# Kernel tuning notes

Hardware: AMD Instinct MI355X
Metric: run time of the kernel (lower is better)

Reference implementation:

```python
import jax, jax.numpy as jnp
import numpy as np

HEAD_DIM = 128
HIDDEN = 2048
MAX_SEQ = 2048
NUM_HEADS = 16
NUM_KV_HEADS = 8
NUM_LAYERS = 32
LAYER_IDX = 5
SCALE = 1.0 / HEAD_DIM ** 0.5
N_REP = NUM_HEADS // NUM_KV_HEADS


def setup_inputs() -> dict:
    key = jax.random.key(0)
    ks = jax.random.split(key, 6)
    x = jax.random.normal(ks[0], (1, HIDDEN, 1, 1), jnp.float32)
    kv_cache = jax.random.normal(ks[1], (2 * NUM_LAYERS, NUM_KV_HEADS, MAX_SEQ, HEAD_DIM), jnp.float32)
    q_w = jax.random.normal(ks[2], (NUM_HEADS * HEAD_DIM, HIDDEN), jnp.float32) * 0.02
    k_w = jax.random.normal(ks[3], (NUM_KV_HEADS * HEAD_DIM, HIDDEN), jnp.float32) * 0.02
    v_w = jax.random.normal(ks[4], (NUM_KV_HEADS * HEAD_DIM, HIDDEN), jnp.float32) * 0.02
    o_w = jax.random.normal(ks[5], (HIDDEN, NUM_HEADS * HEAD_DIM), jnp.float32) * 0.02
    return {"x": x, "kv_cache": kv_cache, "q_w": q_w, "k_w": k_w, "v_w": v_w,
            "o_w": o_w, "current_pos": 1024}


def reference(x, kv_cache, q_w, k_w, v_w, o_w, current_pos):
    # 1x1 Conv2d on [1, C, 1, 1] == matrix-vector product
    xv = x.reshape(HIDDEN)
    q = (q_w @ xv).reshape(NUM_HEADS, HEAD_DIM)        # [H, D]
    k = (k_w @ xv).reshape(NUM_KV_HEADS, HEAD_DIM)     # [KV, D]
    v = (v_w @ xv).reshape(NUM_KV_HEADS, HEAD_DIM)     # [KV, D]

    k_idx = 2 * LAYER_IDX
    v_idx = k_idx + 1
    # functional slice-write of the new token's K/V into the cache
    kv_cache = kv_cache.at[k_idx, :, current_pos, :].set(k)
    kv_cache = kv_cache.at[v_idx, :, current_pos, :].set(v)

    k_full = kv_cache[k_idx]   # [KV, S, D]
    v_full = kv_cache[v_idx]   # [KV, S, D]

    # GQA: q head h uses kv head h // N_REP (matches repeat+view in torch)
    qg = q.reshape(NUM_KV_HEADS, N_REP, HEAD_DIM)                     # [KV, R, D]
    scores = jnp.einsum('grd,gsd->grs', qg, k_full) * SCALE           # [KV, R, S]
    probs = jax.nn.softmax(scores, axis=-1)
    attn = jnp.einsum('grs,gsd->grd', probs, v_full)                  # [KV, R, D]
    attn = attn.reshape(NUM_HEADS * HEAD_DIM)

    out = (o_w @ attn).reshape(1, HIDDEN, 1, 1)
    return out
```

## Files before the change

### kernel.cpp

```cpp
#include <hip/hip_runtime.h>

#define HEAD_DIM   128
#define HIDDEN     2048
#define MAX_SEQ    2048
#define NUM_HEADS  16
#define NUM_KV     8
#define LAYER_IDX  5
#define NSPLIT     16
#define CHUNK      128
#define SCALE      0.08838834764831845f

#define WS_Q     0
#define WS_K     2048
#define WS_V     3072
#define WS_LP    4096
#define WS_OP    4352

__device__ __forceinline__ float wave_reduce_sum(float v) {
    #pragma unroll
    for (int off = 32; off > 0; off >>= 1) v += __shfl_xor(v, off);
    return v;
}

__global__ __launch_bounds__(256) void qkv_kernel(const float* __restrict__ x,
                                                  const float* __restrict__ q_w,
                                                  const float* __restrict__ k_w,
                                                  const float* __restrict__ v_w,
                                                  float* __restrict__ ws) {
    const int t  = threadIdx.x;
    const int r0 = blockIdx.x * 4;
    float4 x0 = ((const float4*)x)[t];
    float4 x1 = ((const float4*)x)[t + 256];

    const float* w0; int obase; float s_out;
    if (r0 < 2048)      { w0 = q_w + (size_t)r0 * HIDDEN;          obase = WS_Q + r0;          s_out = SCALE; }
    else if (r0 < 3072) { w0 = k_w + (size_t)(r0 - 2048) * HIDDEN; obase = WS_K + (r0 - 2048); s_out = 1.0f; }
    else                { w0 = v_w + (size_t)(r0 - 3072) * HIDDEN; obase = WS_V + (r0 - 3072); s_out = 1.0f; }

    float p[4];
    #pragma unroll
    for (int r = 0; r < 4; ++r) {
        const float* w = w0 + (size_t)r * HIDDEN;
        float4 a0 = ((const float4*)w)[t];
        float4 a1 = ((const float4*)w)[t + 256];
        p[r] = a0.x * x0.x + a0.y * x0.y + a0.z * x0.z + a0.w * x0.w
             + a1.x * x1.x + a1.y * x1.y + a1.z * x1.z + a1.w * x1.w;
    }
    #pragma unroll
    for (int r = 0; r < 4; ++r) p[r] = wave_reduce_sum(p[r]);

    __shared__ float red[4][4];
    const int wave = t >> 6, lane = t & 63;
    if (lane == 0) {
        #pragma unroll
        for (int r = 0; r < 4; ++r) red[r][wave] = p[r];
    }
    __syncthreads();
    if (t < 4) ws[obase + t] = (red[t][0] + red[t][1] + red[t][2] + red[t][3]) * s_out;
}

__global__ __launch_bounds__(256) void attn_kernel(const float* __restrict__ kv_cache,
                                                   const float* __restrict__ wsq,
                                                   const int* __restrict__ cur_pos,
                                                   float* __restrict__ lp,
                                                   float* __restrict__ op) {
    const int g     = blockIdx.x;
    const int split = blockIdx.y;
    const int s0    = split * CHUNK;
    const int cpos  = *cur_pos;
    const int t     = threadIdx.x;
    const int wave  = t >> 6, lane = t & 63;

    const float* kbase = kv_cache + ((size_t)(2 * LAYER_IDX)     * NUM_KV + g) * (size_t)MAX_SEQ * HEAD_DIM;
    const float* vbase = kv_cache + ((size_t)(2 * LAYER_IDX + 1) * NUM_KV + g) * (size_t)MAX_SEQ * HEAD_DIM;
    const float* knew  = wsq + WS_K + g * HEAD_DIM;
    const float* vnew  = wsq + WS_V + g * HEAD_DIM;

    __shared__ float4 tile[CHUNK * 32];
    __shared__ float  sc[2][CHUNK];
    __shared__ float4 smv[2][8][32];
    __shared__ float  lred[2][2];
    __shared__ float  lsum[2];

    const int dq = lane & 3;
    float4 q0s[8], q1s[8];
    {
        const float4* q04 = (const float4*)(wsq + WS_Q + (g * 2 + 0) * HEAD_DIM);
        const float4* q14 = (const float4*)(wsq + WS_Q + (g * 2 + 1) * HEAD_DIM);
        #pragma unroll
        for (int r = 0; r < 8; ++r) { q0s[r] = q04[dq * 8 + r]; q1s[r] = q14[dq * 8 + r]; }
    }

    #pragma unroll
    for (int i = 0; i < 16; ++i) {
        const int idx = i * 256 + t;
        const int row = idx >> 5, col = idx & 31;
        const int s = s0 + row;
        const float4* src = (s == cpos) ? (const float4*)knew
                                        : (const float4*)(kbase + (size_t)s * HEAD_DIM);
        tile[idx] = src[col];
    }
    __syncthreads();

    #pragma unroll
    for (int p = 0; p < 2; ++p) {
        const int pos = p * 64 + wave * 16 + (lane >> 2);
        float a0 = 0.f, a1 = 0.f;
        #pragma unroll
        for (int r = 0; r < 8; ++r) {
            float4 kk = tile[pos * 32 + dq * 8 + r];
            a0 += q0s[r].x * kk.x + q0s[r].y * kk.y + q0s[r].z * kk.z + q0s[r].w * kk.w;
            a1 += q1s[r].x * kk.x + q1s[r].y * kk.y + q1s[r].z * kk.z + q1s[r].w * kk.w;
        }
        a0 += __shfl_xor(a0, 1); a0 += __shfl_xor(a0, 2);
        a1 += __shfl_xor(a1, 1); a1 += __shfl_xor(a1, 2);
        if (dq == 0) { sc[0][pos] = a0; sc[1][pos] = a1; }
    }
    __syncthreads();

    if (t < 128) {
        float e0 = __expf(sc[0][t]);
        float e1 = __expf(sc[1][t]);
        sc[0][t] = e0; sc[1][t] = e1;
        float w0 = wave_reduce_sum(e0);
        float w1 = wave_reduce_sum(e1);
        if (lane == 0) { lred[0][wave] = w0; lred[1][wave] = w1; }
    }
    __syncthreads();
    if (t == 0) {
        lsum[0] = lred[0][0] + lred[0][1];
        lsum[1] = lred[1][0] + lred[1][1];
    }

    __syncthreads();
    #pragma unroll
    for (int i = 0; i < 16; ++i) {
        const int idx = i * 256 + t;
        const int row = idx >> 5, col = idx & 31;
        const int s = s0 + row;
        const float4* src = (s == cpos) ? (const float4*)vnew
                                        : (const float4*)(vbase + (size_t)s * HEAD_DIM);
        tile[idx] = src[col];
    }
    __syncthreads();

    {
        const int d4 = t & 31, subrow = t >> 5;
        float4 a0 = {0.f,0.f,0.f,0.f}, a1 = {0.f,0.f,0.f,0.f};
        #pragma unroll
        for (int i = 0; i < 16; ++i) {
            const int j = i * 8 + subrow;
            float4 vv = tile[j * 32 + d4];
            const float e0 = sc[0][j], e1 = sc[1][j];
            a0.x += e0 * vv.x; a0.y += e0 * vv.y; a0.z += e0 * vv.z; a0.w += e0 * vv.w;
            a1.x += e1 * vv.x; a1.y += e1 * vv.y; a1.z += e1 * vv.z; a1.w += e1 * vv.w;
        }
        smv[0][subrow][d4] = a0;
        smv[1][subrow][d4] = a1;
    }
    __syncthreads();
    if (t < 64) {
        const int rep = t >> 5, q4 = t & 31;
        float4 s = smv[rep][0][q4];
        #pragma unroll
        for (int r = 1; r < 8; ++r) {
            float4 b = smv[rep][r][q4];
            s.x += b.x; s.y += b.y; s.z += b.z; s.w += b.w;
        }
        const int h = g * 2 + rep;
        ((float4*)(op + ((size_t)(h * NSPLIT + split)) * HEAD_DIM))[q4] = s;
    }
    if (t == 0) {
        lp[(g * 2 + 0) * NSPLIT + split] = lsum[0];
        lp[(g * 2 + 1) * NSPLIT + split] = lsum[1];
    }
}

__global__ __launch_bounds__(256) void out_kernel(const float* __restrict__ o_w,
                                                  const float* __restrict__ lp,
                                                  const float* __restrict__ op,
                                                  float* __restrict__ out) {
    const int t = threadIdx.x;
    __shared__ float  linv[NUM_HEADS];
    __shared__ float4 attn_s[512];
    __shared__ float  red[8][4];

    if (t < NUM_HEADS) {
        float l = 0.f;
        #pragma unroll
        for (int s = 0; s < NSPLIT; ++s) l += lp[t * NSPLIT + s];
        linv[t] = 1.0f / l;
    }
    __syncthreads();

    const float4* op4 = (const float4*)op;
    #pragma unroll
    for (int k = 0; k < 2; ++k) {
        const int fi = t + 256 * k;
        const int h = fi >> 5, d4 = fi & 31;
        float4 acc = {0.f,0.f,0.f,0.f};
        #pragma unroll
        for (int s = 0; s < NSPLIT; ++s) {
            float4 v = op4[(h * NSPLIT + s) * 32 + d4];
            acc.x += v.x; acc.y += v.y; acc.z += v.z; acc.w += v.w;
        }
        const float li = linv[h];
        acc.x *= li; acc.y *= li; acc.z *= li; acc.w *= li;
        attn_s[fi] = acc;
    }
    __syncthreads();

    const int row0 = blockIdx.x * 8;
    float4 xa0 = attn_s[t];
    float4 xa1 = attn_s[t + 256];

    float p[8];
    #pragma unroll
    for (int r = 0; r < 8; ++r) {
        const float* w = o_w + (size_t)(row0 + r) * HIDDEN;
        float4 a0 = ((const float4*)w)[t];
        float4 a1 = ((const float4*)w)[t + 256];
        p[r] = a0.x * xa0.x + a0.y * xa0.y + a0.z * xa0.z + a0.w * xa0.w
             + a1.x * xa1.x + a1.y * xa1.y + a1.z * xa1.z + a1.w * xa1.w;
    }
    #pragma unroll
    for (int r = 0; r < 8; ++r) p[r] = wave_reduce_sum(p[r]);

    const int wave = t >> 6, lane = t & 63;
    if (lane == 0) {
        #pragma unroll
        for (int r = 0; r < 8; ++r) red[r][wave] = p[r];
    }
    __syncthreads();
    if (t < 8) out[row0 + t] = red[t][0] + red[t][1] + red[t][2] + red[t][3];
}

extern "C" void kernel_launch(void* const* d_in, const int* in_sizes, int n_in,
                              void* d_out, int out_size, void* d_ws, size_t ws_size,
                              hipStream_t stream) {
    const float* x    = (const float*)d_in[0];
    const float* kv   = (const float*)d_in[1];
    const float* q_w  = (const float*)d_in[2];
    const float* k_w  = (const float*)d_in[3];
    const float* v_w  = (const float*)d_in[4];
    const float* o_w  = (const float*)d_in[5];
    const int*   cpos = (const int*)d_in[6];
    float* ws  = (float*)d_ws;
    float* out = (float*)d_out;

    qkv_kernel<<<1024, 256, 0, stream>>>(x, q_w, k_w, v_w, ws);
    attn_kernel<<<dim3(NUM_KV, NSPLIT), 256, 0, stream>>>(kv, ws, cpos, ws + WS_LP, ws + WS_OP);
    out_kernel<<<256, 256, 0, stream>>>(o_w, ws + WS_LP, ws + WS_OP, out);
}
```

Before: 25.43 us.

## Stream K/V directly from global in attention, widen blocks, double QKV rows per block

The attention kernel drops the shared-memory K and V tiles and has each thread read its K row and V rows straight from global memory, running 512 threads per block so the 128 positions are covered in one pass. This removes two tile-staging phases and their barriers, and lets the V loads start without waiting for a full tile copy. The QKV projection now computes 8 rows per block over half as many blocks, and the output kernel reduces the split sums with shuffles instead of a serial loop. The trade-offs are that K and V reads are now less coalesced across the wave and the QKV kernel has fewer blocks, which lowers occupancy.

```diff
diff --git a/kernel.cpp b/kernel.cpp
--- a/kernel.cpp
+++ b/kernel.cpp
@@ -28,7 +28,7 @@
                                                   const float* __restrict__ v_w,
                                                   float* __restrict__ ws) {
     const int t  = threadIdx.x;
-    const int r0 = blockIdx.x * 4;
+    const int r0 = blockIdx.x * 8;
     float4 x0 = ((const float4*)x)[t];
     float4 x1 = ((const float4*)x)[t + 256];
 
@@ -37,9 +37,9 @@
     else if (r0 < 3072) { w0 = k_w + (size_t)(r0 - 2048) * HIDDEN; obase = WS_K + (r0 - 2048); s_out = 1.0f; }
     else                { w0 = v_w + (size_t)(r0 - 3072) * HIDDEN; obase = WS_V + (r0 - 3072); s_out = 1.0f; }
 
-    float p[4];
-    #pragma unroll
-    for (int r = 0; r < 4; ++r) {
+    float p[8];
+    #pragma unroll
+    for (int r = 0; r < 8; ++r) {
         const float* w = w0 + (size_t)r * HIDDEN;
         float4 a0 = ((const float4*)w)[t];
         float4 a1 = ((const float4*)w)[t + 256];
@@ -47,19 +47,19 @@
              + a1.x * x1.x + a1.y * x1.y + a1.z * x1.z + a1.w * x1.w;
     }
     #pragma unroll
-    for (int r = 0; r < 4; ++r) p[r] = wave_reduce_sum(p[r]);
-
-    __shared__ float red[4][4];
+    for (int r = 0; r < 8; ++r) p[r] = wave_reduce_sum(p[r]);
+
+    __shared__ float red[8][4];
     const int wave = t >> 6, lane = t & 63;
     if (lane == 0) {
         #pragma unroll
-        for (int r = 0; r < 4; ++r) red[r][wave] = p[r];
-    }
-    __syncthreads();
-    if (t < 4) ws[obase + t] = (red[t][0] + red[t][1] + red[t][2] + red[t][3]) * s_out;
-}
-
-__global__ __launch_bounds__(256) void attn_kernel(const float* __restrict__ kv_cache,
+        for (int r = 0; r < 8; ++r) red[r][wave] = p[r];
+    }
+    __syncthreads();
+    if (t < 8) ws[obase + t] = (red[t][0] + red[t][1] + red[t][2] + red[t][3]) * s_out;
+}
+
+__global__ __launch_bounds__(512) void attn_kernel(const float* __restrict__ kv_cache,
                                                    const float* __restrict__ wsq,
                                                    const int* __restrict__ cur_pos,
                                                    float* __restrict__ lp,
@@ -76,41 +76,26 @@
     const float* knew  = wsq + WS_K + g * HEAD_DIM;
     const float* vnew  = wsq + WS_V + g * HEAD_DIM;
 
-    __shared__ float4 tile[CHUNK * 32];
     __shared__ float  sc[2][CHUNK];
-    __shared__ float4 smv[2][8][32];
-    __shared__ float  lred[2][2];
-    __shared__ float  lsum[2];
-
-    const int dq = lane & 3;
-    float4 q0s[8], q1s[8];
+    __shared__ float4 smv[2][16][32];
+    __shared__ float  lred4[4];
+
     {
+        const int dq  = lane & 3;
+        const int pos = wave * 16 + (lane >> 2);
+        const int s   = s0 + pos;
+        const float4* krow = (s == cpos) ? (const float4*)knew
+                                         : (const float4*)(kbase + (size_t)s * HEAD_DIM);
         const float4* q04 = (const float4*)(wsq + WS_Q + (g * 2 + 0) * HEAD_DIM);
         const float4* q14 = (const float4*)(wsq + WS_Q + (g * 2 + 1) * HEAD_DIM);
-        #pragma unroll
-        for (int r = 0; r < 8; ++r) { q0s[r] = q04[dq * 8 + r]; q1s[r] = q14[dq * 8 + r]; }
-    }
-
-    #pragma unroll
-    for (int i = 0; i < 16; ++i) {
-        const int idx = i * 256 + t;
-        const int row = idx >> 5, col = idx & 31;
-        const int s = s0 + row;
-        const float4* src = (s == cpos) ? (const float4*)knew
-                                        : (const float4*)(kbase + (size_t)s * HEAD_DIM);
-        tile[idx] = src[col];
-    }
-    __syncthreads();
-
-    #pragma unroll
-    for (int p = 0; p < 2; ++p) {
-        const int pos = p * 64 + wave * 16 + (lane >> 2);
         float a0 = 0.f, a1 = 0.f;
         #pragma unroll
         for (int r = 0; r < 8; ++r) {
-            float4 kk = tile[pos * 32 + dq * 8 + r];
-            a0 += q0s[r].x * kk.x + q0s[r].y * kk.y + q0s[r].z * kk.z + q0s[r].w * kk.w;
-            a1 += q1s[r].x * kk.x + q1s[r].y * kk.y + q1s[r].z * kk.z + q1s[r].w * kk.w;
+            float4 kk = krow[dq * 8 + r];
+            float4 qa = q04[dq * 8 + r];
+            float4 qb = q14[dq * 8 + r];
+            a0 += qa.x * kk.x + qa.y * kk.y + qa.z * kk.z + qa.w * kk.w;
+            a1 += qb.x * kk.x + qb.y * kk.y + qb.z * kk.z + qb.w * kk.w;
         }
         a0 += __shfl_xor(a0, 1); a0 += __shfl_xor(a0, 2);
         a1 += __shfl_xor(a1, 1); a1 += __shfl_xor(a1, 2);
@@ -118,29 +103,12 @@
     }
     __syncthreads();
 
-    if (t < 128) {
-        float e0 = __expf(sc[0][t]);
-        float e1 = __expf(sc[1][t]);
-        sc[0][t] = e0; sc[1][t] = e1;
-        float w0 = wave_reduce_sum(e0);
-        float w1 = wave_reduce_sum(e1);
-        if (lane == 0) { lred[0][wave] = w0; lred[1][wave] = w1; }
-    }
-    __syncthreads();
-    if (t == 0) {
-        lsum[0] = lred[0][0] + lred[0][1];
-        lsum[1] = lred[1][0] + lred[1][1];
-    }
-
-    __syncthreads();
-    #pragma unroll
-    for (int i = 0; i < 16; ++i) {
-        const int idx = i * 256 + t;
-        const int row = idx >> 5, col = idx & 31;
-        const int s = s0 + row;
-        const float4* src = (s == cpos) ? (const float4*)vnew
-                                        : (const float4*)(vbase + (size_t)s * HEAD_DIM);
-        tile[idx] = src[col];
+    if (t < 256) {
+        const int rr = t >> 7, j = t & 127;
+        float e = __expf(sc[rr][j]);
+        sc[rr][j] = e;
+        float l = wave_reduce_sum(e);
+        if (lane == 0) lred4[wave] = l;
     }
     __syncthreads();
 
@@ -148,9 +116,11 @@
         const int d4 = t & 31, subrow = t >> 5;
         float4 a0 = {0.f,0.f,0.f,0.f}, a1 = {0.f,0.f,0.f,0.f};
         #pragma unroll
-        for (int i = 0; i < 16; ++i) {
-            const int j = i * 8 + subrow;
-            float4 vv = tile[j * 32 + d4];
+        for (int i = 0; i < 8; ++i) {
+            const int j = i * 16 + subrow;
+            const int s = s0 + j;
+            const float* vrow = (s == cpos) ? vnew : (vbase + (size_t)s * HEAD_DIM);
+            float4 vv = ((const float4*)vrow)[d4];
             const float e0 = sc[0][j], e1 = sc[1][j];
             a0.x += e0 * vv.x; a0.y += e0 * vv.y; a0.z += e0 * vv.z; a0.w += e0 * vv.w;
             a1.x += e1 * vv.x; a1.y += e1 * vv.y; a1.z += e1 * vv.z; a1.w += e1 * vv.w;
@@ -163,7 +133,7 @@
         const int rep = t >> 5, q4 = t & 31;
         float4 s = smv[rep][0][q4];
         #pragma unroll
-        for (int r = 1; r < 8; ++r) {
+        for (int r = 1; r < 16; ++r) {
             float4 b = smv[rep][r][q4];
             s.x += b.x; s.y += b.y; s.z += b.z; s.w += b.w;
         }
@@ -171,8 +141,8 @@
         ((float4*)(op + ((size_t)(h * NSPLIT + split)) * HEAD_DIM))[q4] = s;
     }
     if (t == 0) {
-        lp[(g * 2 + 0) * NSPLIT + split] = lsum[0];
-        lp[(g * 2 + 1) * NSPLIT + split] = lsum[1];
+        lp[(g * 2 + 0) * NSPLIT + split] = lred4[0] + lred4[1];
+        lp[(g * 2 + 1) * NSPLIT + split] = lred4[2] + lred4[3];
     }
 }
 
@@ -185,11 +155,11 @@
     __shared__ float4 attn_s[512];
     __shared__ float  red[8][4];
 
-    if (t < NUM_HEADS) {
-        float l = 0.f;
-        #pragma unroll
-        for (int s = 0; s < NSPLIT; ++s) l += lp[t * NSPLIT + s];
-        linv[t] = 1.0f / l;
+    {
+        float l = lp[t];
+        #pragma unroll
+        for (int off = 1; off < 16; off <<= 1) l += __shfl_xor(l, off);
+        if ((t & 15) == 0) linv[t >> 4] = 1.0f / l;
     }
     __syncthreads();
 
@@ -248,7 +218,7 @@
     float* ws  = (float*)d_ws;
     float* out = (float*)d_out;
 
-    qkv_kernel<<<1024, 256, 0, stream>>>(x, q_w, k_w, v_w, ws);
-    attn_kernel<<<dim3(NUM_KV, NSPLIT), 256, 0, stream>>>(kv, ws, cpos, ws + WS_LP, ws + WS_OP);
+    qkv_kernel<<<512, 256, 0, stream>>>(x, q_w, k_w, v_w, ws);
+    attn_kernel<<<dim3(NUM_KV, NSPLIT), 512, 0, stream>>>(kv, ws, cpos, ws + WS_LP, ws + WS_OP);
     out_kernel<<<256, 256, 0, stream>>>(o_w, ws + WS_LP, ws + WS_OP, out);
 }
```

New measurement: 26.98 us. 1.06x slower.

## Issue K and V chunk loads together into registers before scoring

Applied to the files above, without the earlier changes.

Loads the K and V chunks for each split into registers up front, so both global loads are in flight at once, instead of loading V only after the softmax step. K is still staged through shared memory for the dot products. V now stays in registers and feeds the weighted sum directly, which removes the second tile fill and two barriers. In exchange each thread holds 32 extra float4 values, raising register pressure and possibly lowering occupancy.

```diff
diff --git a/kernel.cpp b/kernel.cpp
--- a/kernel.cpp
+++ b/kernel.cpp
@@ -76,21 +76,13 @@
     const float* knew  = wsq + WS_K + g * HEAD_DIM;
     const float* vnew  = wsq + WS_V + g * HEAD_DIM;
 
-    __shared__ float4 tile[CHUNK * 32];
+    __shared__ float4 ktile[CHUNK * 32];
     __shared__ float  sc[2][CHUNK];
     __shared__ float4 smv[2][8][32];
     __shared__ float  lred[2][2];
     __shared__ float  lsum[2];
 
-    const int dq = lane & 3;
-    float4 q0s[8], q1s[8];
-    {
-        const float4* q04 = (const float4*)(wsq + WS_Q + (g * 2 + 0) * HEAD_DIM);
-        const float4* q14 = (const float4*)(wsq + WS_Q + (g * 2 + 1) * HEAD_DIM);
-        #pragma unroll
-        for (int r = 0; r < 8; ++r) { q0s[r] = q04[dq * 8 + r]; q1s[r] = q14[dq * 8 + r]; }
-    }
-
+    float4 kreg[16];
     #pragma unroll
     for (int i = 0; i < 16; ++i) {
         const int idx = i * 256 + t;
@@ -98,23 +90,45 @@
         const int s = s0 + row;
         const float4* src = (s == cpos) ? (const float4*)knew
                                         : (const float4*)(kbase + (size_t)s * HEAD_DIM);
-        tile[idx] = src[col];
-    }
-    __syncthreads();
-
-    #pragma unroll
-    for (int p = 0; p < 2; ++p) {
-        const int pos = p * 64 + wave * 16 + (lane >> 2);
-        float a0 = 0.f, a1 = 0.f;
-        #pragma unroll
-        for (int r = 0; r < 8; ++r) {
-            float4 kk = tile[pos * 32 + dq * 8 + r];
-            a0 += q0s[r].x * kk.x + q0s[r].y * kk.y + q0s[r].z * kk.z + q0s[r].w * kk.w;
-            a1 += q1s[r].x * kk.x + q1s[r].y * kk.y + q1s[r].z * kk.z + q1s[r].w * kk.w;
-        }
-        a0 += __shfl_xor(a0, 1); a0 += __shfl_xor(a0, 2);
-        a1 += __shfl_xor(a1, 1); a1 += __shfl_xor(a1, 2);
-        if (dq == 0) { sc[0][pos] = a0; sc[1][pos] = a1; }
+        kreg[i] = src[col];
+    }
+
+    const int vd4 = t & 31, vsub = t >> 5;
+    float4 vreg[16];
+    #pragma unroll
+    for (int i = 0; i < 16; ++i) {
+        const int j = i * 8 + vsub;
+        const int s = s0 + j;
+        const float* vrow = (s == cpos) ? vnew : (vbase + (size_t)s * HEAD_DIM);
+        vreg[i] = ((const float4*)vrow)[vd4];
+    }
+
+    #pragma unroll
+    for (int i = 0; i < 16; ++i) ktile[i * 256 + t] = kreg[i];
+    __syncthreads();
+
+    const int dq = lane & 3;
+    {
+        const float4* q04 = (const float4*)(wsq + WS_Q + (g * 2 + 0) * HEAD_DIM);
+        const float4* q14 = (const float4*)(wsq + WS_Q + (g * 2 + 1) * HEAD_DIM);
+        float4 q0s[8], q1s[8];
+        #pragma unroll
+        for (int r = 0; r < 8; ++r) { q0s[r] = q04[dq * 8 + r]; q1s[r] = q14[dq * 8 + r]; }
+
+        #pragma unroll
+        for (int p = 0; p < 2; ++p) {
+            const int pos = p * 64 + wave * 16 + (lane >> 2);
+            float a0 = 0.f, a1 = 0.f;
+            #pragma unroll
+            for (int r = 0; r < 8; ++r) {
+                float4 kk = ktile[pos * 32 + dq * 8 + r];
+                a0 += q0s[r].x * kk.x + q0s[r].y * kk.y + q0s[r].z * kk.z + q0s[r].w * kk.w;
+                a1 += q1s[r].x * kk.x + q1s[r].y * kk.y + q1s[r].z * kk.z + q1s[r].w * kk.w;
+            }
+            a0 += __shfl_xor(a0, 1); a0 += __shfl_xor(a0, 2);
+            a1 += __shfl_xor(a1, 1); a1 += __shfl_xor(a1, 2);
+            if (dq == 0) { sc[0][pos] = a0; sc[1][pos] = a1; }
+        }
     }
     __syncthreads();
 
@@ -132,31 +146,18 @@
         lsum[1] = lred[1][0] + lred[1][1];
     }
 
-    __syncthreads();
-    #pragma unroll
-    for (int i = 0; i < 16; ++i) {
-        const int idx = i * 256 + t;
-        const int row = idx >> 5, col = idx & 31;
-        const int s = s0 + row;
-        const float4* src = (s == cpos) ? (const float4*)vnew
-                                        : (const float4*)(vbase + (size_t)s * HEAD_DIM);
-        tile[idx] = src[col];
-    }
-    __syncthreads();
-
     {
-        const int d4 = t & 31, subrow = t >> 5;
         float4 a0 = {0.f,0.f,0.f,0.f}, a1 = {0.f,0.f,0.f,0.f};
         #pragma unroll
         for (int i = 0; i < 16; ++i) {
-            const int j = i * 8 + subrow;
-            float4 vv = tile[j * 32 + d4];
+            const int j = i * 8 + vsub;
             const float e0 = sc[0][j], e1 = sc[1][j];
+            const float4 vv = vreg[i];
             a0.x += e0 * vv.x; a0.y += e0 * vv.y; a0.z += e0 * vv.z; a0.w += e0 * vv.w;
             a1.x += e1 * vv.x; a1.y += e1 * vv.y; a1.z += e1 * vv.z; a1.w += e1 * vv.w;
         }
-        smv[0][subrow][d4] = a0;
-        smv[1][subrow][d4] = a1;
+        smv[0][vsub][vd4] = a0;
+        smv[1][vsub][vd4] = a1;
     }
     __syncthreads();
     if (t < 64) {
```

After: 25.25 us, median of 2. About the same (-0.7%).
